# Optimization experiments

Hardware: AMD Instinct MI355X
Metric: run time of the kernel (lower is better)

Reference implementation:

```python
import jax, jax.numpy as jnp
import numpy as np
import math

# ---- real-basis Wigner 3j via nullspace of rotation generators ----

def _su2_gen(l):
    m = np.arange(-l, l + 1)
    jz = np.diag(m).astype(complex)
    jp = np.zeros((2 * l + 1, 2 * l + 1), complex)
    for i, mm in enumerate(m[:-1]):
        jp[i + 1, i] = math.sqrt(l * (l + 1) - mm * (mm + 1))
    jm = jp.conj().T
    return (jp + jm) / 2, (jp - jm) / 2j, jz


def _c2r(l):
    # complex -> real spherical-harmonic change of basis
    U = np.zeros((2 * l + 1, 2 * l + 1), complex)
    U[l, l] = 1.0
    s = 1 / math.sqrt(2)
    for m in range(1, l + 1):
        U[l + m, l + m] = (-1) ** m * s
        U[l + m, l - m] = s
        U[l - m, l - m] = 1j * s
        U[l - m, l + m] = -1j * (-1) ** m * s
    return U


def _real_gens(l):
    U = _c2r(l)
    return [np.real(U @ (-1j * J) @ U.conj().T) for J in _su2_gen(l)]


_W3J_CACHE = {}

def _w3j(l1, l2, l3):
    key = (l1, l2, l3)
    if key in _W3J_CACHE:
        return _W3J_CACHE[key]
    X1, X2, X3 = _real_gens(l1), _real_gens(l2), _real_gens(l3)
    d1, d2, d3 = 2 * l1 + 1, 2 * l2 + 1, 2 * l3 + 1
    I1, I2, I3 = np.eye(d1), np.eye(d2), np.eye(d3)
    blocks = []
    for a in range(3):
        K = (np.kron(np.kron(X1[a], I2), I3)
             + np.kron(np.kron(I1, X2[a]), I3)
             + np.kron(np.kron(I1, I2), X3[a]))
        blocks.append(K)
    M = np.concatenate(blocks, 0)
    _, _, Vh = np.linalg.svd(M)
    v = Vh[-1]
    if v[np.argmax(np.abs(v))] < 0:
        v = -v
    w = (v / np.linalg.norm(v)).reshape(d1, d2, d3)
    _W3J_CACHE[key] = w
    return w


# ---- replicate WeightedTensorProduct.__init__ layout logic ----

def _build(ls1, ls2, ls_out):
    dim = lambda ls: sum(2 * l + 1 for l in ls)
    d1, d2, do = dim(ls1), dim(ls2), dim(ls_out)
    lmax2 = max(ls2)
    max_l3 = max(ls_out) + 1
    layout = {}
    idx1 = 0
    for l1 in ls1:
        idx2 = 0
        for l2 in ls2:
            for l3 in range(abs(l1 - l2), min(l1 + l2 + 1, max_l3)):
                layout.setdefault(l3, []).append((l1, l2, idx1 * d2 + idx2))
            idx2 += 2 * l2 + 1
        idx1 += 2 * l1 + 1
    l3s = sorted(layout)
    cbh = sum((2 * l3 + 1) * len(layout[l3]) for l3 in l3s)
    cb = np.zeros((cbh, d1 * d2), np.float32)
    row = 0
    for l3 in l3s:
        layout[l3] = sorted(layout[l3], key=lambda x: x[0] * lmax2 + x[1])
        for (l1, l2, col) in layout[l3]:
            w = _w3j(l1, l2, l3) * math.sqrt(2 * l3 + 1)  # (2l1+1, 2l2+1, 2l3+1)
            for m1 in range(2 * l1 + 1):
                cb[row:row + 2 * l3 + 1, col + m1 * d2: col + m1 * d2 + 2 * l2 + 1] = w[m1].T
            row += 2 * l3 + 1
    # weight-tying mask (one scalar weight per (out-irrep, cb-path) pair)
    out_mult = {}
    for l in ls_out:
        out_mult[l] = out_mult.get(l, 0) + 1
    rows_idx, cols_idx = [], []
    row_idx, widx = 0, 0
    for ol3 in sorted(out_mult):
        for _ in range(out_mult[ol3]):
            col_idx = 0
            for l3 in l3s:
                for _m in range(len(layout[l3])):
                    if ol3 == l3:
                        for m in range(2 * l3 + 1):
                            rows_idx.append((row_idx + m) * cbh + col_idx + m)
                            cols_idx.append(widx)
                        widx += 1
                    col_idx += 2 * l3 + 1
            row_idx += 2 * ol3 + 1
    return cb, np.array(rows_idx, np.int32), np.array(cols_idx, np.int32), widx, do, cbh


def setup_inputs() -> dict:
    LS = [0] * 8 + [1] * 8 + [2] * 4  # dim = 52, for in1, in2 and out
    cb, rows, cols, nw, do, H = _build(LS, LS, LS)
    d = sum(2 * l + 1 for l in LS)
    rng = np.random.default_rng(0)
    w = rng.standard_normal(nw).astype(np.float32)
    Wf = np.zeros(do * H, np.float32)
    Wf[rows] = w[cols]
    B = 4096
    k1, k2 = jax.random.split(jax.random.key(0))
    return {
        "in1": jax.random.normal(k1, (B, d), jnp.float32),
        "in2": jax.random.normal(k2, (B, d), jnp.float32),
        "cb_matrix": jnp.asarray(cb),                  # [H, d*d]
        "weight_matrix": jnp.asarray(Wf.reshape(do, H)),  # [do, H]
    }


def reference(in1, in2, cb_matrix, weight_matrix):
    # out = (W @ C @ outer^T)^T  ==  outer @ C^T @ W^T
    B = in1.shape[0]
    outer = (in1[:, :, None] * in2[:, None, :]).reshape(B, -1)  # [B, d1*d2]
    z = outer @ cb_matrix.T                                     # [B, cb_height]
    return z @ weight_matrix.T                                  # [B, dim_out]
```

## Files before the change

kernel.cpp:

```cpp
#include <hip/hip_runtime.h>
#include <hip/hip_bf16.h>

#define D    52
#define DD   2704
#define HH   2000
#define DO   52
#define KP   3328
#define NO   64
#define KS   4
#define KT_TOTAL (KP/32)
#define KT_PER   (KT_TOTAL/KS)
#define MG   16
#define KCH  128
#define WHP  2048

typedef __attribute__((ext_vector_type(8))) short short8;
typedef __attribute__((ext_vector_type(4))) float f32x4;

#define WB_OFF     0
#define WB_BYTES   (NO * WHP * 2)
#define MTP_OFF    (WB_OFF + WB_BYTES)
#define MTP_BYTES  (MG * NO * DD * 4)
#define MTB_OFF    (MTP_OFF + MTP_BYTES)
#define MTB_BYTES  (KT_TOTAL * NO * 32 * 2)
#define OUTP_OFF   (MTB_OFF + MTB_BYTES)
#define OUTP_BYTES (KS * 4096 * NO * 4)

static __device__ __forceinline__ unsigned short f2bf(float f) {
    __hip_bfloat16 h = __float2bfloat16(f);
    return __builtin_bit_cast(unsigned short, h);
}

__global__ __launch_bounds__(256) void k_packw(
    const float* __restrict__ W, unsigned short* __restrict__ Wb) {
    int idx = blockIdx.x * 256 + threadIdx.x;
    if (idx >= NO * WHP) return;
    int o = idx >> 11, h = idx & (WHP - 1);
    float v = (o < DO && h < HH) ? W[o * HH + h] : 0.f;
    Wb[idx] = f2bf(v);
}

__global__ __launch_bounds__(256) void k_mgemm(
    const float* __restrict__ cb, const unsigned short* __restrict__ Wb,
    float* __restrict__ mtp) {
    __shared__ float shAT[64][33];
    int lane = threadIdx.x & 63;
    int w    = __builtin_amdgcn_readfirstlane(threadIdx.x >> 6);
    int r    = lane & 15;
    int kg   = lane >> 4;
    int ij0  = blockIdx.x * 64;
    int g    = blockIdx.y;

    f32x4 acc[4];
#pragma unroll
    for (int mt = 0; mt < 4; ++mt) acc[mt] = (f32x4){0.f, 0.f, 0.f, 0.f};

    int srow = threadIdx.x >> 6;
    int scol = threadIdx.x & 63;
    int sij  = ij0 + scol;
    bool ijv = (sij < DD);

#pragma unroll
    for (int kt = 0; kt < KCH / 32; ++kt) {
        int h0 = g * KCH + kt * 32;
        __syncthreads();
#pragma unroll
        for (int p = 0; p < 8; ++p) {
            int row = srow + p * 4;
            int h = h0 + row;
            float v = (h < HH && ijv) ? cb[(size_t)h * DD + sij] : 0.f;
            shAT[scol][row] = v;
        }
        __syncthreads();

        short8 bf;
#pragma unroll
        for (int e = 0; e < 8; ++e)
            bf[e] = (short)f2bf(shAT[w * 16 + r][kg * 8 + e]);
#pragma unroll
        for (int mt = 0; mt < 4; ++mt) {
            short8 a = *reinterpret_cast<const short8*>(
                Wb + (size_t)(mt * 16 + r) * WHP + g * KCH + kt * 32 + kg * 8);
            acc[mt] = __builtin_amdgcn_mfma_f32_16x16x32_bf16(a, bf, acc[mt], 0, 0, 0);
        }
    }

    int ij = ij0 + w * 16 + r;
    if (ij < DD) {
#pragma unroll
        for (int mt = 0; mt < 4; ++mt) {
#pragma unroll
            for (int q = 0; q < 4; ++q) {
                int o = mt * 16 + kg * 4 + q;
                mtp[((size_t)g * NO + o) * DD + ij] = acc[mt][q];
            }
        }
    }
}

__global__ __launch_bounds__(256) void k_reduce_mtb(
    const float* __restrict__ mtp, unsigned short* __restrict__ mtB) {
    int k = blockIdx.x * 256 + threadIdx.x;
    int o = blockIdx.y;
    int i = k >> 6, j = k & 63;
    float s = 0.f;
    if (j < D) {
        size_t base = (size_t)o * DD + i * D + j;
#pragma unroll
        for (int g = 0; g < MG; ++g) s += mtp[(size_t)g * (NO * DD) + base];
    }
    mtB[((size_t)(k >> 5) * NO + o) * 32 + ((k >> 3) & 3) * 8 + (k & 7)] = f2bf(s);
}

__global__ __launch_bounds__(256) void k_main_mfma(
    const float* __restrict__ in1, const float* __restrict__ in2,
    const unsigned short* __restrict__ mtB, float* __restrict__ outp) {
    __shared__ float sh1[16][53];
    __shared__ float sh2[16][69];

    int lane = threadIdx.x & 63;
    int wv   = __builtin_amdgcn_readfirstlane(threadIdx.x >> 6);
    int b0   = blockIdx.x * 16;
    int ks   = blockIdx.y;
    int o0   = wv * 16;

    for (int t = threadIdx.x; t < 16 * 64; t += 256) {
        int r = t >> 6, j = t & 63;
        sh2[r][j] = (j < D) ? in2[(size_t)(b0 + r) * D + j] : 0.f;
    }
    for (int t = threadIdx.x; t < 16 * D; t += 256) {
        int r = t / D, i = t - r * D;
        sh1[r][i] = in1[(size_t)(b0 + r) * D + i];
    }
    __syncthreads();

    int r  = lane & 15;
    int kg = lane >> 4;
    const unsigned short* bp =
        mtB + ((size_t)(ks * KT_PER) * NO + o0 + r) * 32 + kg * 8;

    f32x4 acc = {0.f, 0.f, 0.f, 0.f};
#pragma unroll 2
    for (int t = 0; t < KT_PER; ++t) {
        int kt   = ks * KT_PER + t;
        int i    = kt >> 1;
        int j0   = (kt & 1) * 32 + kg * 8;
        float f1 = sh1[r][i];
        short8 a;
#pragma unroll
        for (int e = 0; e < 8; ++e)
            a[e] = (short)f2bf(f1 * sh2[r][j0 + e]);
        short8 b = *reinterpret_cast<const short8*>(bp + (size_t)t * (NO * 32));
        acc = __builtin_amdgcn_mfma_f32_16x16x32_bf16(a, b, acc, 0, 0, 0);
    }

#pragma unroll
    for (int q = 0; q < 4; ++q) {
        int row = kg * 4 + q;
        outp[((size_t)ks * 4096 + b0 + row) * NO + o0 + r] = acc[q];
    }
}

__global__ __launch_bounds__(256) void k_out(
    const float* __restrict__ outp, float* __restrict__ out, int B) {
    int idx = blockIdx.x * 256 + threadIdx.x;
    if (idx >= B * DO) return;
    int b = idx / DO, o = idx - b * DO;
    float s = 0.f;
#pragma unroll
    for (int g = 0; g < KS; ++g) s += outp[((size_t)g * B + b) * NO + o];
    out[idx] = s;
}

extern "C" void kernel_launch(void* const* d_in, const int* in_sizes, int n_in,
                              void* d_out, int out_size, void* d_ws, size_t ws_size,
                              hipStream_t stream) {
    const float* in1 = (const float*)d_in[0];
    const float* in2 = (const float*)d_in[1];
    const float* cb  = (const float*)d_in[2];
    const float* W   = (const float*)d_in[3];
    float* out = (float*)d_out;

    int B = in_sizes[0] / D;

    char* ws = (char*)d_ws;
    unsigned short* Wb   = (unsigned short*)(ws + WB_OFF);
    float*          mtp  = (float*)(ws + MTP_OFF);
    unsigned short* mtB  = (unsigned short*)(ws + MTB_OFF);
    float*          outp = (float*)(ws + OUTP_OFF);

    hipLaunchKernelGGL(k_packw, dim3((NO * WHP + 255) / 256), dim3(256), 0,
                       stream, W, Wb);
    hipLaunchKernelGGL(k_mgemm, dim3((DD + 63) / 64, MG), dim3(256), 0,
                       stream, cb, Wb, mtp);
    hipLaunchKernelGGL(k_reduce_mtb, dim3(KP / 256, NO), dim3(256), 0,
                       stream, mtp, mtB);
    hipLaunchKernelGGL(k_main_mfma, dim3(B / 16, KS), dim3(256), 0,
                       stream, in1, in2, mtB, outp);
    hipLaunchKernelGGL(k_out, dim3((B * DO + 255) / 256), dim3(256), 0,
                       stream, outp, out, B);
}
```

Measured before the change: 106.6 us.

## Retile main MFMA kernel so each wave builds A once and reuses it across N

The main kernel now processes 64 batch rows per block, with each wave owning 16 rows and computing all 64 outputs. Each bf16 A fragment (the outer product of in1 and in2) is built once and reused across four MFMAs instead of being rebuilt per output tile. Input staging uses float4 loads, and A-operand reads from shared memory are vectorised. Split-K is doubled and the M-precompute group count halved with a larger chunk, which changes the grid shapes and the workspace partial sizes. The trade-off is more register pressure and fewer blocks along the batch dimension.

```diff
diff --git a/kernel.cpp b/kernel.cpp
--- a/kernel.cpp
+++ b/kernel.cpp
@@ -7,11 +7,11 @@
 #define DO   52
 #define KP   3328
 #define NO   64
-#define KS   4
+#define KS   8
 #define KT_TOTAL (KP/32)
 #define KT_PER   (KT_TOTAL/KS)
-#define MG   16
-#define KCH  128
+#define MG   8
+#define KCH  256
 #define WHP  2048
 
 typedef __attribute__((ext_vector_type(8))) short short8;
@@ -115,49 +115,70 @@
 __global__ __launch_bounds__(256) void k_main_mfma(
     const float* __restrict__ in1, const float* __restrict__ in2,
     const unsigned short* __restrict__ mtB, float* __restrict__ outp) {
-    __shared__ float sh1[16][53];
-    __shared__ float sh2[16][69];
+    __shared__ float sh1[64][53];
+    __shared__ float sh2[64][72];
 
     int lane = threadIdx.x & 63;
-    int wv   = __builtin_amdgcn_readfirstlane(threadIdx.x >> 6);
-    int b0   = blockIdx.x * 16;
+    int w    = __builtin_amdgcn_readfirstlane(threadIdx.x >> 6);
+    int b0   = blockIdx.x * 64;
     int ks   = blockIdx.y;
-    int o0   = wv * 16;
-
-    for (int t = threadIdx.x; t < 16 * 64; t += 256) {
-        int r = t >> 6, j = t & 63;
-        sh2[r][j] = (j < D) ? in2[(size_t)(b0 + r) * D + j] : 0.f;
-    }
-    for (int t = threadIdx.x; t < 16 * D; t += 256) {
-        int r = t / D, i = t - r * D;
-        sh1[r][i] = in1[(size_t)(b0 + r) * D + i];
+    int r    = lane & 15;
+    int kg   = lane >> 4;
+
+    for (int t = threadIdx.x; t < 64 * 13; t += 256) {
+        int row = t / 13, q = t - row * 13;
+        float4 v = *reinterpret_cast<const float4*>(in2 + (size_t)(b0 + row) * D + 4 * q);
+        sh2[row][4 * q + 0] = v.x; sh2[row][4 * q + 1] = v.y;
+        sh2[row][4 * q + 2] = v.z; sh2[row][4 * q + 3] = v.w;
+    }
+    for (int t = threadIdx.x; t < 64 * 12; t += 256) {
+        int row = t / 12, j = 52 + (t - row * 12);
+        sh2[row][j] = 0.f;
+    }
+    for (int t = threadIdx.x; t < 64 * 13; t += 256) {
+        int row = t / 13, q = t - row * 13;
+        float4 v = *reinterpret_cast<const float4*>(in1 + (size_t)(b0 + row) * D + 4 * q);
+        sh1[row][4 * q + 0] = v.x; sh1[row][4 * q + 1] = v.y;
+        sh1[row][4 * q + 2] = v.z; sh1[row][4 * q + 3] = v.w;
     }
     __syncthreads();
 
-    int r  = lane & 15;
-    int kg = lane >> 4;
-    const unsigned short* bp =
-        mtB + ((size_t)(ks * KT_PER) * NO + o0 + r) * 32 + kg * 8;
-
-    f32x4 acc = {0.f, 0.f, 0.f, 0.f};
-#pragma unroll 2
+    int mrow = w * 16 + r;
+    f32x4 acc[4];
+#pragma unroll
+    for (int nt = 0; nt < 4; ++nt) acc[nt] = (f32x4){0.f, 0.f, 0.f, 0.f};
+
+    const unsigned short* bbase =
+        mtB + ((size_t)(ks * KT_PER) * NO + r) * 32 + kg * 8;
+
+#pragma unroll 4
     for (int t = 0; t < KT_PER; ++t) {
         int kt   = ks * KT_PER + t;
         int i    = kt >> 1;
         int j0   = (kt & 1) * 32 + kg * 8;
-        float f1 = sh1[r][i];
+        float f1 = sh1[mrow][i];
+        float4 v0 = *reinterpret_cast<const float4*>(&sh2[mrow][j0]);
+        float4 v1 = *reinterpret_cast<const float4*>(&sh2[mrow][j0 + 4]);
         short8 a;
-#pragma unroll
-        for (int e = 0; e < 8; ++e)
-            a[e] = (short)f2bf(f1 * sh2[r][j0 + e]);
-        short8 b = *reinterpret_cast<const short8*>(bp + (size_t)t * (NO * 32));
-        acc = __builtin_amdgcn_mfma_f32_16x16x32_bf16(a, b, acc, 0, 0, 0);
-    }
-
-#pragma unroll
-    for (int q = 0; q < 4; ++q) {
-        int row = kg * 4 + q;
-        outp[((size_t)ks * 4096 + b0 + row) * NO + o0 + r] = acc[q];
+        a[0] = (short)f2bf(f1 * v0.x); a[1] = (short)f2bf(f1 * v0.y);
+        a[2] = (short)f2bf(f1 * v0.z); a[3] = (short)f2bf(f1 * v0.w);
+        a[4] = (short)f2bf(f1 * v1.x); a[5] = (short)f2bf(f1 * v1.y);
+        a[6] = (short)f2bf(f1 * v1.z); a[7] = (short)f2bf(f1 * v1.w);
+#pragma unroll
+        for (int nt = 0; nt < 4; ++nt) {
+            short8 b = *reinterpret_cast<const short8*>(
+                bbase + ((size_t)t * NO + nt * 16) * 32);
+            acc[nt] = __builtin_amdgcn_mfma_f32_16x16x32_bf16(a, b, acc[nt], 0, 0, 0);
+        }
+    }
+
+#pragma unroll
+    for (int nt = 0; nt < 4; ++nt) {
+#pragma unroll
+        for (int q = 0; q < 4; ++q) {
+            outp[((size_t)ks * 4096 + b0 + w * 16 + kg * 4 + q) * NO + nt * 16 + r]
+                = acc[nt][q];
+        }
     }
 }
 
@@ -195,7 +216,7 @@
                        stream, cb, Wb, mtp);
     hipLaunchKernelGGL(k_reduce_mtb, dim3(KP / 256, NO), dim3(256), 0,
                        stream, mtp, mtB);
-    hipLaunchKernelGGL(k_main_mfma, dim3(B / 16, KS), dim3(256), 0,
+    hipLaunchKernelGGL(k_main_mfma, dim3(B / 64, KS), dim3(256), 0,
                        stream, in1, in2, mtB, outp);
     hipLaunchKernelGGL(k_out, dim3((B * DO + 255) / 256), dim3(256), 0,
                        stream, outp, out, B);
```

After: 114.7 us. 1.08x slower.
